# Kernel optimization log

Measured on AMD Instinct MI355X. Metric: run time of the kernel, lower is better.

The kernel has to match this reference:

```python
import jax, jax.numpy as jnp
import numpy as np

N = 50000      # nodes
E = 800000     # edges
F_IN = 128     # in_channels
H = 128        # hidden_channels
C = 10         # num_classes
G = 512        # graphs in batch
EPS = 1e-5     # batchnorm eps


def setup_inputs() -> dict:
    key = jax.random.key(0)
    ks = jax.random.split(key, 18)
    s = 0.05
    return {
        "x": jax.random.normal(ks[0], (N, F_IN), jnp.float32),
        "edge_index": jax.random.randint(ks[1], (2, E), 0, N, dtype=jnp.int32),
        "batch": jnp.sort(jax.random.randint(ks[2], (N,), 0, G, dtype=jnp.int32)),
        "W1": jax.random.normal(ks[3], (F_IN, H), jnp.float32) * s,
        "b1": jnp.zeros((H,), jnp.float32),
        "gamma1": jnp.ones((H,), jnp.float32),
        "beta1": jnp.zeros((H,), jnp.float32),
        "mean1": jax.random.normal(ks[4], (H,), jnp.float32) * 0.1,
        "var1": jax.random.uniform(ks[5], (H,), jnp.float32, 0.5, 1.5),
        "W2": jax.random.normal(ks[6], (H, H), jnp.float32) * s,
        "b2": jnp.zeros((H,), jnp.float32),
        "gamma2": jnp.ones((H,), jnp.float32),
        "beta2": jnp.zeros((H,), jnp.float32),
        "mean2": jax.random.normal(ks[7], (H,), jnp.float32) * 0.1,
        "var2": jax.random.uniform(ks[8], (H,), jnp.float32, 0.5, 1.5),
        "Wlin": jax.random.normal(ks[9], (H, C), jnp.float32) * s,
        "blin": jnp.zeros((C,), jnp.float32),
    }


def _gcn_conv(x, W, b, src, dst):
    # GCNConv with add_self_loops=True, symmetric normalization.
    h = x @ W                                             # [N, H]
    deg = jax.ops.segment_sum(jnp.ones((E,), h.dtype), dst, num_segments=N) + 1.0
    dis = jax.lax.rsqrt(deg)                              # deg^{-1/2}, [N]
    norm = dis[src] * dis[dst]                            # [E]
    agg = jax.ops.segment_sum(h[src] * norm[:, None], dst, num_segments=N)
    agg = agg + h * (dis * dis)[:, None]                  # self-loop term
    return agg + b


def _bn_eval(x, gamma, beta, mean, var):
    return gamma * (x - mean) * jax.lax.rsqrt(var + EPS) + beta


def reference(x, edge_index, batch, W1, b1, gamma1, beta1, mean1, var1,
              W2, b2, gamma2, beta2, mean2, var2, Wlin, blin):
    src, dst = edge_index[0], edge_index[1]
    h = _gcn_conv(x, W1, b1, src, dst)
    h = jax.nn.relu(_bn_eval(h, gamma1, beta1, mean1, var1))
    # dropout: identity in eval mode
    h = _gcn_conv(h, W2, b2, src, dst)
    h = jax.nn.relu(_bn_eval(h, gamma2, beta2, mean2, var2))
    # global_mean_pool over graph ids
    sums = jax.ops.segment_sum(h, batch, num_segments=G)          # [G, H]
    cnts = jax.ops.segment_sum(jnp.ones((N,), h.dtype), batch, num_segments=G)
    pooled = sums / jnp.maximum(cnts, 1.0)[:, None]
    return pooled @ Wlin + blin                                   # [G, C]
```

## Files before the change

kernel.cpp:

```cpp
#include <hip/hip_runtime.h>
#include <hip/hip_bf16.h>

#define N_NODES 50000
#define N_EDGES 800000
#define HDIM 128
#define NGRAPH 512
#define NCLS 10
#define BN_EPS 1e-5f
#define MAXDEG 64

typedef unsigned int  uint32;
typedef unsigned short ushort16;

__device__ inline float2 bf2f(uint32 u) {
    return make_float2(__uint_as_float(u << 16), __uint_as_float(u & 0xffff0000u));
}
__device__ inline ushort16 f2bf(float f) {
    uint32 u = __float_as_uint(f);
    u += 0x7fffu + ((u >> 16) & 1u);
    return (ushort16)(u >> 16);
}
__device__ inline uint32 packbf2(float lo, float hi) {
    return (uint32)f2bf(lo) | ((uint32)f2bf(hi) << 16);
}


#define GEMM1_BLOCKS 1563
#define FRONT_GRID (3 * GEMM1_BLOCKS)

__global__ __launch_bounds__(256) void front(const float* __restrict__ x,
                                             const float* __restrict__ W1,
                                             ushort16* __restrict__ bufA,
                                             const int* __restrict__ src,
                                             const int* __restrict__ dst,
                                             int* __restrict__ deg,
                                             int* __restrict__ epad)
{
    __shared__ float xs[32][36];
    __shared__ float ws[32][128];
    const int tid = threadIdx.x;
    const int grp = blockIdx.x / 3, rem = blockIdx.x % 3;

    if (rem != 0) {
        int e = (grp * 2 + (rem - 1)) * 256 + tid;
        if (e < N_EDGES) {
            int d   = dst[e];
            int pos = atomicAdd(&deg[d], 1);
            epad[(size_t)d * MAXDEG + pos] = src[e];
        }
        return;
    }

    const int row0 = grp * 32;
    const int tx   = tid & 31;
    const int ty   = tid >> 5;

    float acc[4][4];
    #pragma unroll
    for (int i = 0; i < 4; ++i)
        #pragma unroll
        for (int j = 0; j < 4; ++j) acc[i][j] = 0.f;

    const int lr = tid >> 3;
    const int lk = (tid & 7) << 2;
    const int wr = tid >> 5;
    const int wc = (tid & 31) << 2;

    for (int k0 = 0; k0 < 128; k0 += 32) {
        float4 xv = make_float4(0.f, 0.f, 0.f, 0.f);
        int grow = row0 + lr;
        if (grow < N_NODES) xv = *(const float4*)(x + (size_t)grow * HDIM + k0 + lk);
        xs[lr][lk] = xv.x; xs[lr][lk + 1] = xv.y; xs[lr][lk + 2] = xv.z; xs[lr][lk + 3] = xv.w;
        #pragma unroll
        for (int i = 0; i < 4; ++i) {
            int kk = wr + i * 8;
            *(float4*)&ws[kk][wc] = *(const float4*)(W1 + (size_t)(k0 + kk) * HDIM + wc);
        }
        __syncthreads();
        #pragma unroll
        for (int kk = 0; kk < 32; kk += 4) {
            float4 wv[4];
            #pragma unroll
            for (int j = 0; j < 4; ++j) wv[j] = *(const float4*)&ws[kk + j][tx << 2];
            #pragma unroll
            for (int i = 0; i < 4; ++i) {
                float4 xr = *(const float4*)&xs[ty * 4 + i][kk];
                acc[i][0] += xr.x * wv[0].x; acc[i][1] += xr.x * wv[0].y;
                acc[i][2] += xr.x * wv[0].z; acc[i][3] += xr.x * wv[0].w;
                acc[i][0] += xr.y * wv[1].x; acc[i][1] += xr.y * wv[1].y;
                acc[i][2] += xr.y * wv[1].z; acc[i][3] += xr.y * wv[1].w;
                acc[i][0] += xr.z * wv[2].x; acc[i][1] += xr.z * wv[2].y;
                acc[i][2] += xr.z * wv[2].z; acc[i][3] += xr.z * wv[2].w;
                acc[i][0] += xr.w * wv[3].x; acc[i][1] += xr.w * wv[3].y;
                acc[i][2] += xr.w * wv[3].z; acc[i][3] += xr.w * wv[3].w;
            }
        }
        __syncthreads();
    }
    #pragma unroll
    for (int i = 0; i < 4; ++i) {
        int grow = row0 + ty * 4 + i;
        if (grow < N_NODES) {
            uint2 o;
            o.x = packbf2(acc[i][0], acc[i][1]);
            o.y = packbf2(acc[i][2], acc[i][3]);
            *(uint2*)(bufA + (size_t)grow * HDIM + (tx << 2)) = o;
        }
    }
}

__global__ __launch_bounds__(256) void rsqrt_deg(const int* __restrict__ deg_i,
                                                 float* __restrict__ dis, int n)
{
    int i = blockIdx.x * 256 + threadIdx.x;
    if (i < n) dis[i] = rsqrtf((float)deg_i[i] + 1.0f);
}

__global__ __launch_bounds__(256) void gemm2_nk128(const ushort16* __restrict__ X,
                                                   const float* __restrict__ W,
                                                   ushort16* __restrict__ Y, int nrows)
{
    __shared__ float xs[32][36];
    __shared__ float ws[32][128];
    const int t    = threadIdx.x;
    const int row0 = blockIdx.x * 32;
    const int tx   = t & 31;
    const int ty   = t >> 5;

    float acc[4][4];
    #pragma unroll
    for (int i = 0; i < 4; ++i)
        #pragma unroll
        for (int j = 0; j < 4; ++j) acc[i][j] = 0.f;

    const int lr = t >> 3;
    const int lk = (t & 7) << 2;
    const int wr = t >> 5;
    const int wc = (t & 31) << 2;

    for (int k0 = 0; k0 < 128; k0 += 32) {
        float4 xv = make_float4(0.f, 0.f, 0.f, 0.f);
        int grow = row0 + lr;
        if (grow < nrows) {
            uint2 u = *(const uint2*)(X + (size_t)grow * HDIM + k0 + lk);
            float2 a = bf2f(u.x), bb = bf2f(u.y);
            xv = make_float4(a.x, a.y, bb.x, bb.y);
        }
        xs[lr][lk] = xv.x; xs[lr][lk + 1] = xv.y; xs[lr][lk + 2] = xv.z; xs[lr][lk + 3] = xv.w;
        #pragma unroll
        for (int i = 0; i < 4; ++i) {
            int kk = wr + i * 8;
            *(float4*)&ws[kk][wc] = *(const float4*)(W + (size_t)(k0 + kk) * HDIM + wc);
        }
        __syncthreads();
        #pragma unroll
        for (int kk = 0; kk < 32; kk += 4) {
            float4 wv[4];
            #pragma unroll
            for (int j = 0; j < 4; ++j) wv[j] = *(const float4*)&ws[kk + j][tx << 2];
            #pragma unroll
            for (int i = 0; i < 4; ++i) {
                float4 xr = *(const float4*)&xs[ty * 4 + i][kk];
                acc[i][0] += xr.x * wv[0].x; acc[i][1] += xr.x * wv[0].y;
                acc[i][2] += xr.x * wv[0].z; acc[i][3] += xr.x * wv[0].w;
                acc[i][0] += xr.y * wv[1].x; acc[i][1] += xr.y * wv[1].y;
                acc[i][2] += xr.y * wv[1].z; acc[i][3] += xr.y * wv[1].w;
                acc[i][0] += xr.z * wv[2].x; acc[i][1] += xr.z * wv[2].y;
                acc[i][2] += xr.z * wv[2].z; acc[i][3] += xr.z * wv[2].w;
                acc[i][0] += xr.w * wv[3].x; acc[i][1] += xr.w * wv[3].y;
                acc[i][2] += xr.w * wv[3].z; acc[i][3] += xr.w * wv[3].w;
            }
        }
        __syncthreads();
    }
    #pragma unroll
    for (int i = 0; i < 4; ++i) {
        int grow = row0 + ty * 4 + i;
        if (grow < nrows) {
            uint2 o;
            o.x = packbf2(acc[i][0], acc[i][1]);
            o.y = packbf2(acc[i][2], acc[i][3]);
            *(uint2*)(Y + (size_t)grow * HDIM + (tx << 2)) = o;
        }
    }
}

__global__ __launch_bounds__(256) void gather_bn_relu(const ushort16* __restrict__ h,
                                                      const int* __restrict__ epad,
                                                      const int* __restrict__ deg,
                                                      const float* __restrict__ dis,
                                                      const float* __restrict__ b,
                                                      const float* __restrict__ gamma,
                                                      const float* __restrict__ beta,
                                                      const float* __restrict__ mean,
                                                      const float* __restrict__ var,
                                                      ushort16* __restrict__ out, int n)
{
    int node = blockIdx.x * 4 + (threadIdx.x >> 6);
    int lane = threadIdx.x & 63;
    if (node >= n) return;
    const int q    = lane >> 4;
    const int ci   = (lane & 15) << 3;
    const int cnt_e = deg[node];
    const int base  = node * MAXDEG;
    const float dd  = dis[node];

    int   s_all  = 0;
    float nm_all = 0.f;
    if (lane < cnt_e) {
        s_all  = epad[base + lane];
        nm_all = dis[s_all] * dd;
    }

    float acc[8] = {0.f, 0.f, 0.f, 0.f, 0.f, 0.f, 0.f, 0.f};
    for (int j = q; j < cnt_e; j += 4) {
        int   s  = __shfl(s_all, j);
        float nm = __shfl(nm_all, j);
        uint4 v  = *(const uint4*)(h + (size_t)s * HDIM + ci);
        float2 f0 = bf2f(v.x), f1 = bf2f(v.y), f2 = bf2f(v.z), f3 = bf2f(v.w);
        acc[0] += f0.x * nm; acc[1] += f0.y * nm;
        acc[2] += f1.x * nm; acc[3] += f1.y * nm;
        acc[4] += f2.x * nm; acc[5] += f2.y * nm;
        acc[6] += f3.x * nm; acc[7] += f3.y * nm;
    }
    #pragma unroll
    for (int k = 0; k < 8; ++k) {
        acc[k] += __shfl_xor(acc[k], 16);
        acc[k] += __shfl_xor(acc[k], 32);
    }

    if (q == 0) {
        uint4 hv = *(const uint4*)(h + (size_t)node * HDIM + ci);
        float2 g0 = bf2f(hv.x), g1 = bf2f(hv.y), g2 = bf2f(hv.z), g3 = bf2f(hv.w);
        float a[8] = {acc[0] + g0.x * dd * dd, acc[1] + g0.y * dd * dd,
                      acc[2] + g1.x * dd * dd, acc[3] + g1.y * dd * dd,
                      acc[4] + g2.x * dd * dd, acc[5] + g2.y * dd * dd,
                      acc[6] + g3.x * dd * dd, acc[7] + g3.y * dd * dd};
        float o[8];
        #pragma unroll
        for (int k = 0; k < 8; ++k) {
            int c = ci + k;
            float sc = gamma[c] * rsqrtf(var[c] + BN_EPS);
            float r  = (a[k] + b[c] - mean[c]) * sc + beta[c];
            o[k] = fmaxf(r, 0.f);
        }
        uint4 ov;
        ov.x = packbf2(o[0], o[1]); ov.y = packbf2(o[2], o[3]);
        ov.z = packbf2(o[4], o[5]); ov.w = packbf2(o[6], o[7]);
        *(uint4*)(out + (size_t)node * HDIM + ci) = ov;
    }
}

__global__ __launch_bounds__(128) void pool_sum(const ushort16* __restrict__ h,
                                                const int* __restrict__ batch,
                                                float* __restrict__ sums,
                                                float* __restrict__ cnt, int n)
{
    int c  = threadIdx.x;
    int n0 = blockIdx.x * 32;
    if (n0 >= n) return;
    int nend = min(n0 + 32, n);
    int curg = batch[n0];
    float acc = 0.f;
    int run = 0;
    for (int i = n0; i < nend; ++i) {
        int g   = batch[i];
        float v = __uint_as_float((uint32)h[(size_t)i * HDIM + c] << 16);
        if (g != curg) {
            atomicAdd(&sums[(size_t)curg * HDIM + c], acc);
            if (c == 0) atomicAdd(&cnt[curg], (float)run);
            acc = 0.f; run = 0; curg = g;
        }
        acc += v; run++;
    }
    atomicAdd(&sums[(size_t)curg * HDIM + c], acc);
    if (c == 0) atomicAdd(&cnt[curg], (float)run);
}

__global__ __launch_bounds__(128) void final_lin(const float* __restrict__ sums,
                                                 const float* __restrict__ cnt,
                                                 const float* __restrict__ Wlin,
                                                 const float* __restrict__ blin,
                                                 float* __restrict__ out)
{
    __shared__ float red[NCLS][2];
    int g = blockIdx.x;
    int t = threadIdx.x;
    float ic = 1.f / fmaxf(cnt[g], 1.f);
    float v  = sums[(size_t)g * HDIM + t] * ic;
    float p[NCLS];
    #pragma unroll
    for (int c = 0; c < NCLS; ++c) p[c] = v * Wlin[t * NCLS + c];
    #pragma unroll
    for (int c = 0; c < NCLS; ++c) {
        float x = p[c];
        for (int off = 32; off > 0; off >>= 1) x += __shfl_down(x, off);
        if ((t & 63) == 0) red[c][t >> 6] = x;
    }
    __syncthreads();
    if (t < NCLS) out[g * NCLS + t] = red[t][0] + red[t][1] + blin[t];
}

extern "C" void kernel_launch(void* const* d_in, const int* in_sizes, int n_in,
                              void* d_out, int out_size, void* d_ws, size_t ws_size,
                              hipStream_t stream)
{
    const float* x     = (const float*)d_in[0];
    const int*   ei    = (const int*)d_in[1];
    const int*   srcp  = ei;
    const int*   dstp  = ei + N_EDGES;
    const int*   batch = (const int*)d_in[2];
    const float* W1    = (const float*)d_in[3];
    const float* b1    = (const float*)d_in[4];
    const float* g1    = (const float*)d_in[5];
    const float* be1   = (const float*)d_in[6];
    const float* m1    = (const float*)d_in[7];
    const float* v1    = (const float*)d_in[8];
    const float* W2    = (const float*)d_in[9];
    const float* b2    = (const float*)d_in[10];
    const float* g2    = (const float*)d_in[11];
    const float* be2   = (const float*)d_in[12];
    const float* m2    = (const float*)d_in[13];
    const float* v2    = (const float*)d_in[14];
    const float* Wlin  = (const float*)d_in[15];
    const float* blin  = (const float*)d_in[16];
    float*       out   = (float*)d_out;

    ushort16* bufA = (ushort16*)d_ws;
    ushort16* bufB = bufA + (size_t)N_NODES * HDIM;
    int*   epad = (int*)(bufB + (size_t)N_NODES * HDIM);
    int*   deg  = epad + (size_t)N_NODES * MAXDEG;
    float* cnt  = (float*)(deg + N_NODES);
    float* sums = cnt + NGRAPH;
    float* dis  = sums + (size_t)NGRAPH * HDIM;

    hipMemsetAsync(deg, 0,
                   (N_NODES + NGRAPH + (size_t)NGRAPH * HDIM) * sizeof(float), stream);

    front<<<FRONT_GRID, 256, 0, stream>>>(x, W1, bufA, srcp, dstp, deg, epad);
    rsqrt_deg<<<(N_NODES + 255) / 256, 256, 0, stream>>>(deg, dis, N_NODES);

    const int gather_blocks = (N_NODES + 3) / 4;

    gather_bn_relu<<<gather_blocks, 256, 0, stream>>>(bufA, epad, deg, dis,
                                                      b1, g1, be1, m1, v1, bufB, N_NODES);
    gemm2_nk128<<<(N_NODES + 31) / 32, 256, 0, stream>>>(bufB, W2, bufA, N_NODES);
    gather_bn_relu<<<gather_blocks, 256, 0, stream>>>(bufA, epad, deg, dis,
                                                      b2, g2, be2, m2, v2, bufB, N_NODES);
    pool_sum<<<(N_NODES + 31) / 32, 128, 0, stream>>>(bufB, batch, sums, cnt, N_NODES);
    final_lin<<<NGRAPH, 128, 0, stream>>>(sums, cnt, Wlin, blin, out);
}
```

Measured before the change: 279.7 us.

## Fuse layer-1 gather with GEMM2 and layer-2 gather with mean pooling

Merges the first aggregation+BN+ReLU with the second GEMM, keeping the 32 aggregated rows in shared memory instead of writing and re-reading them from global memory. Likewise merges the second aggregation with the graph pooling so the final node features never reach global memory. This removes two kernel launches and two full N×128 bf16 round trips. In exchange, gather blocks now cover 32 nodes each (8 per wave, serial), which lowers parallelism and latency hiding in the gather phase, and shared memory use per block grows.

Result: no change. 283.3 us (+1.3%).

```diff
diff --git a/kernel.cpp b/kernel.cpp
--- a/kernel.cpp
+++ b/kernel.cpp
@@ -23,10 +23,14 @@
 __device__ inline uint32 packbf2(float lo, float hi) {
     return (uint32)f2bf(lo) | ((uint32)f2bf(hi) << 16);
 }
+__device__ inline float bfround(float f) {
+    return __uint_as_float((uint32)f2bf(f) << 16);
+}
 
 
 #define GEMM1_BLOCKS 1563
 #define FRONT_GRID (3 * GEMM1_BLOCKS)
+#define AB_BLOCKS 1563
 
 __global__ __launch_bounds__(256) void front(const float* __restrict__ x,
                                              const float* __restrict__ W1,
@@ -116,89 +120,18 @@
     if (i < n) dis[i] = rsqrtf((float)deg_i[i] + 1.0f);
 }
 
-__global__ __launch_bounds__(256) void gemm2_nk128(const ushort16* __restrict__ X,
-                                                   const float* __restrict__ W,
-                                                   ushort16* __restrict__ Y, int nrows)
-{
-    __shared__ float xs[32][36];
-    __shared__ float ws[32][128];
-    const int t    = threadIdx.x;
-    const int row0 = blockIdx.x * 32;
-    const int tx   = t & 31;
-    const int ty   = t >> 5;
-
-    float acc[4][4];
-    #pragma unroll
-    for (int i = 0; i < 4; ++i)
-        #pragma unroll
-        for (int j = 0; j < 4; ++j) acc[i][j] = 0.f;
-
-    const int lr = t >> 3;
-    const int lk = (t & 7) << 2;
-    const int wr = t >> 5;
-    const int wc = (t & 31) << 2;
-
-    for (int k0 = 0; k0 < 128; k0 += 32) {
-        float4 xv = make_float4(0.f, 0.f, 0.f, 0.f);
-        int grow = row0 + lr;
-        if (grow < nrows) {
-            uint2 u = *(const uint2*)(X + (size_t)grow * HDIM + k0 + lk);
-            float2 a = bf2f(u.x), bb = bf2f(u.y);
-            xv = make_float4(a.x, a.y, bb.x, bb.y);
-        }
-        xs[lr][lk] = xv.x; xs[lr][lk + 1] = xv.y; xs[lr][lk + 2] = xv.z; xs[lr][lk + 3] = xv.w;
-        #pragma unroll
-        for (int i = 0; i < 4; ++i) {
-            int kk = wr + i * 8;
-            *(float4*)&ws[kk][wc] = *(const float4*)(W + (size_t)(k0 + kk) * HDIM + wc);
-        }
-        __syncthreads();
-        #pragma unroll
-        for (int kk = 0; kk < 32; kk += 4) {
-            float4 wv[4];
-            #pragma unroll
-            for (int j = 0; j < 4; ++j) wv[j] = *(const float4*)&ws[kk + j][tx << 2];
-            #pragma unroll
-            for (int i = 0; i < 4; ++i) {
-                float4 xr = *(const float4*)&xs[ty * 4 + i][kk];
-                acc[i][0] += xr.x * wv[0].x; acc[i][1] += xr.x * wv[0].y;
-                acc[i][2] += xr.x * wv[0].z; acc[i][3] += xr.x * wv[0].w;
-                acc[i][0] += xr.y * wv[1].x; acc[i][1] += xr.y * wv[1].y;
-                acc[i][2] += xr.y * wv[1].z; acc[i][3] += xr.y * wv[1].w;
-                acc[i][0] += xr.z * wv[2].x; acc[i][1] += xr.z * wv[2].y;
-                acc[i][2] += xr.z * wv[2].z; acc[i][3] += xr.z * wv[2].w;
-                acc[i][0] += xr.w * wv[3].x; acc[i][1] += xr.w * wv[3].y;
-                acc[i][2] += xr.w * wv[3].z; acc[i][3] += xr.w * wv[3].w;
-            }
-        }
-        __syncthreads();
-    }
-    #pragma unroll
-    for (int i = 0; i < 4; ++i) {
-        int grow = row0 + ty * 4 + i;
-        if (grow < nrows) {
-            uint2 o;
-            o.x = packbf2(acc[i][0], acc[i][1]);
-            o.y = packbf2(acc[i][2], acc[i][3]);
-            *(uint2*)(Y + (size_t)grow * HDIM + (tx << 2)) = o;
-        }
-    }
-}
-
-__global__ __launch_bounds__(256) void gather_bn_relu(const ushort16* __restrict__ h,
-                                                      const int* __restrict__ epad,
-                                                      const int* __restrict__ deg,
-                                                      const float* __restrict__ dis,
-                                                      const float* __restrict__ b,
-                                                      const float* __restrict__ gamma,
-                                                      const float* __restrict__ beta,
-                                                      const float* __restrict__ mean,
-                                                      const float* __restrict__ var,
-                                                      ushort16* __restrict__ out, int n)
-{
-    int node = blockIdx.x * 4 + (threadIdx.x >> 6);
-    int lane = threadIdx.x & 63;
-    if (node >= n) return;
+__device__ inline void gather_node_to_lds(const ushort16* __restrict__ h,
+                                          const int* __restrict__ epad,
+                                          const int* __restrict__ deg,
+                                          const float* __restrict__ dis,
+                                          const float* __restrict__ b,
+                                          const float* __restrict__ gamma,
+                                          const float* __restrict__ beta,
+                                          const float* __restrict__ mean,
+                                          const float* __restrict__ var,
+                                          float (*hrow)[HDIM],
+                                          int node, int r, int lane)
+{
     const int q    = lane >> 4;
     const int ci   = (lane & 15) << 3;
     const int cnt_e = deg[node];
@@ -236,45 +169,142 @@
                       acc[2] + g1.x * dd * dd, acc[3] + g1.y * dd * dd,
                       acc[4] + g2.x * dd * dd, acc[5] + g2.y * dd * dd,
                       acc[6] + g3.x * dd * dd, acc[7] + g3.y * dd * dd};
-        float o[8];
         #pragma unroll
         for (int k = 0; k < 8; ++k) {
             int c = ci + k;
             float sc = gamma[c] * rsqrtf(var[c] + BN_EPS);
-            float r  = (a[k] + b[c] - mean[c]) * sc + beta[c];
-            o[k] = fmaxf(r, 0.f);
-        }
-        uint4 ov;
-        ov.x = packbf2(o[0], o[1]); ov.y = packbf2(o[2], o[3]);
-        ov.z = packbf2(o[4], o[5]); ov.w = packbf2(o[6], o[7]);
-        *(uint4*)(out + (size_t)node * HDIM + ci) = ov;
-    }
-}
-
-__global__ __launch_bounds__(128) void pool_sum(const ushort16* __restrict__ h,
-                                                const int* __restrict__ batch,
-                                                float* __restrict__ sums,
-                                                float* __restrict__ cnt, int n)
-{
-    int c  = threadIdx.x;
-    int n0 = blockIdx.x * 32;
-    if (n0 >= n) return;
-    int nend = min(n0 + 32, n);
-    int curg = batch[n0];
-    float acc = 0.f;
-    int run = 0;
-    for (int i = n0; i < nend; ++i) {
-        int g   = batch[i];
-        float v = __uint_as_float((uint32)h[(size_t)i * HDIM + c] << 16);
-        if (g != curg) {
-            atomicAdd(&sums[(size_t)curg * HDIM + c], acc);
-            if (c == 0) atomicAdd(&cnt[curg], (float)run);
-            acc = 0.f; run = 0; curg = g;
-        }
-        acc += v; run++;
-    }
-    atomicAdd(&sums[(size_t)curg * HDIM + c], acc);
-    if (c == 0) atomicAdd(&cnt[curg], (float)run);
+            float rr = (a[k] + b[c] - mean[c]) * sc + beta[c];
+            hrow[r][c] = bfround(fmaxf(rr, 0.f));
+        }
+    }
+}
+
+__global__ __launch_bounds__(256) void gather1_gemm2(const ushort16* __restrict__ h,
+                                                     const int* __restrict__ epad,
+                                                     const int* __restrict__ deg,
+                                                     const float* __restrict__ dis,
+                                                     const float* __restrict__ b,
+                                                     const float* __restrict__ gamma,
+                                                     const float* __restrict__ beta,
+                                                     const float* __restrict__ mean,
+                                                     const float* __restrict__ var,
+                                                     const float* __restrict__ W2,
+                                                     ushort16* __restrict__ Y, int n)
+{
+    __shared__ float hrow[32][HDIM];
+    __shared__ float ws[32][128];
+    const int tid  = threadIdx.x;
+    const int wave = tid >> 6, lane = tid & 63;
+    const int node0 = blockIdx.x * 32;
+
+    #pragma unroll 1
+    for (int it = 0; it < 8; ++it) {
+        int r = wave * 8 + it;
+        int node = node0 + r;
+        if (node < n)
+            gather_node_to_lds(h, epad, deg, dis, b, gamma, beta, mean, var,
+                               hrow, node, r, lane);
+    }
+    __syncthreads();
+
+    const int tx = tid & 31;
+    const int ty = tid >> 5;
+
+    float acc[4][4];
+    #pragma unroll
+    for (int i = 0; i < 4; ++i)
+        #pragma unroll
+        for (int j = 0; j < 4; ++j) acc[i][j] = 0.f;
+
+    const int wr = tid >> 5;
+    const int wc = (tid & 31) << 2;
+
+    for (int k0 = 0; k0 < 128; k0 += 32) {
+        #pragma unroll
+        for (int i = 0; i < 4; ++i) {
+            int kk = wr + i * 8;
+            *(float4*)&ws[kk][wc] = *(const float4*)(W2 + (size_t)(k0 + kk) * HDIM + wc);
+        }
+        __syncthreads();
+        #pragma unroll
+        for (int kk = 0; kk < 32; kk += 4) {
+            float4 wv[4];
+            #pragma unroll
+            for (int j = 0; j < 4; ++j) wv[j] = *(const float4*)&ws[kk + j][tx << 2];
+            #pragma unroll
+            for (int i = 0; i < 4; ++i) {
+                float4 xr = *(const float4*)&hrow[ty * 4 + i][k0 + kk];
+                acc[i][0] += xr.x * wv[0].x; acc[i][1] += xr.x * wv[0].y;
+                acc[i][2] += xr.x * wv[0].z; acc[i][3] += xr.x * wv[0].w;
+                acc[i][0] += xr.y * wv[1].x; acc[i][1] += xr.y * wv[1].y;
+                acc[i][2] += xr.y * wv[1].z; acc[i][3] += xr.y * wv[1].w;
+                acc[i][0] += xr.z * wv[2].x; acc[i][1] += xr.z * wv[2].y;
+                acc[i][2] += xr.z * wv[2].z; acc[i][3] += xr.z * wv[2].w;
+                acc[i][0] += xr.w * wv[3].x; acc[i][1] += xr.w * wv[3].y;
+                acc[i][2] += xr.w * wv[3].z; acc[i][3] += xr.w * wv[3].w;
+            }
+        }
+        __syncthreads();
+    }
+    #pragma unroll
+    for (int i = 0; i < 4; ++i) {
+        int grow = node0 + ty * 4 + i;
+        if (grow < n) {
+            uint2 o;
+            o.x = packbf2(acc[i][0], acc[i][1]);
+            o.y = packbf2(acc[i][2], acc[i][3]);
+            *(uint2*)(Y + (size_t)grow * HDIM + (tx << 2)) = o;
+        }
+    }
+}
+
+__global__ __launch_bounds__(256) void gather2_pool(const ushort16* __restrict__ h,
+                                                    const int* __restrict__ epad,
+                                                    const int* __restrict__ deg,
+                                                    const float* __restrict__ dis,
+                                                    const float* __restrict__ b,
+                                                    const float* __restrict__ gamma,
+                                                    const float* __restrict__ beta,
+                                                    const float* __restrict__ mean,
+                                                    const float* __restrict__ var,
+                                                    const int* __restrict__ batch,
+                                                    float* __restrict__ sums,
+                                                    float* __restrict__ cnt, int n)
+{
+    __shared__ float hrow[32][HDIM];
+    const int tid  = threadIdx.x;
+    const int wave = tid >> 6, lane = tid & 63;
+    const int node0 = blockIdx.x * 32;
+
+    #pragma unroll 1
+    for (int it = 0; it < 8; ++it) {
+        int r = wave * 8 + it;
+        int node = node0 + r;
+        if (node < n)
+            gather_node_to_lds(h, epad, deg, dis, b, gamma, beta, mean, var,
+                               hrow, node, r, lane);
+    }
+    __syncthreads();
+
+    if (tid < 128) {
+        int c = tid;
+        int nvalid = min(node0 + 32, n) - node0;
+        int curg = batch[node0];
+        float acc = 0.f;
+        int run = 0;
+        for (int i = 0; i < nvalid; ++i) {
+            int g   = batch[node0 + i];
+            float v = hrow[i][c];
+            if (g != curg) {
+                atomicAdd(&sums[(size_t)curg * HDIM + c], acc);
+                if (c == 0) atomicAdd(&cnt[curg], (float)run);
+                acc = 0.f; run = 0; curg = g;
+            }
+            acc += v; run++;
+        }
+        atomicAdd(&sums[(size_t)curg * HDIM + c], acc);
+        if (c == 0) atomicAdd(&cnt[curg], (float)run);
+    }
 }
 
 __global__ __launch_bounds__(128) void final_lin(const float* __restrict__ sums,
@@ -340,13 +370,10 @@
     front<<<FRONT_GRID, 256, 0, stream>>>(x, W1, bufA, srcp, dstp, deg, epad);
     rsqrt_deg<<<(N_NODES + 255) / 256, 256, 0, stream>>>(deg, dis, N_NODES);
 
-    const int gather_blocks = (N_NODES + 3) / 4;
-
-    gather_bn_relu<<<gather_blocks, 256, 0, stream>>>(bufA, epad, deg, dis,
-                                                      b1, g1, be1, m1, v1, bufB, N_NODES);
-    gemm2_nk128<<<(N_NODES + 31) / 32, 256, 0, stream>>>(bufB, W2, bufA, N_NODES);
-    gather_bn_relu<<<gather_blocks, 256, 0, stream>>>(bufA, epad, deg, dis,
-                                                      b2, g2, be2, m2, v2, bufB, N_NODES);
-    pool_sum<<<(N_NODES + 31) / 32, 128, 0, stream>>>(bufB, batch, sums, cnt, N_NODES);
+    gather1_gemm2<<<AB_BLOCKS, 256, 0, stream>>>(bufA, epad, deg, dis,
+                                                 b1, g1, be1, m1, v1, W2, bufB, N_NODES);
+    gather2_pool<<<AB_BLOCKS, 256, 0, stream>>>(bufB, epad, deg, dis,
+                                                b2, g2, be2, m2, v2, batch,
+                                                sums, cnt, N_NODES);
     final_lin<<<NGRAPH, 128, 0, stream>>>(sums, cnt, Wlin, blin, out);
 }
```
